# Kernel tuning notes

Hardware: AMD Instinct MI355X
Metric: run time of the kernel (lower is better)

## Reference

```python
import jax, jax.numpy as jnp
import numpy as np

C = 1.0          # curvature of PoincareBall
SQRT_C = 1.0
MIN_NORM = 1e-15
PROJ_EPS = 4e-3  # float32 boundary eps used by PoincareBall.proj
N_NODES = 50000


def _norm(x):
    return jnp.clip(jnp.linalg.norm(x, axis=-1, keepdims=True), MIN_NORM)


def _artanh(x):
    return jnp.arctanh(jnp.clip(x, -1.0 + 1e-7, 1.0 - 1e-7))


def proj(x):
    # clip points to the open ball of radius (1-eps)/sqrt(c)
    norm = _norm(x)
    maxnorm = (1.0 - PROJ_EPS) / SQRT_C
    return jnp.where(norm > maxnorm, x / norm * maxnorm, x)


def expmap0(u):
    u_norm = _norm(u)
    return jnp.tanh(SQRT_C * u_norm) * u / (SQRT_C * u_norm)


def logmap0(p):
    p_norm = _norm(p)
    return _artanh(SQRT_C * p_norm) * p / (SQRT_C * p_norm)


def mobius_add(x, y):
    x2 = jnp.sum(x * x, -1, keepdims=True)
    y2 = jnp.sum(y * y, -1, keepdims=True)
    xy = jnp.sum(x * y, -1, keepdims=True)
    num = (1.0 + 2.0 * C * xy + C * y2) * x + (1.0 - C * x2) * y
    den = 1.0 + 2.0 * C * xy + C * C * x2 * y2
    return num / jnp.clip(den, MIN_NORM)


def mobius_matvec(m, x):
    x_norm = _norm(x)
    mx = x @ m.T  # [N, d_out]
    mx_norm = _norm(mx)
    res = jnp.tanh(mx_norm / x_norm * _artanh(SQRT_C * x_norm)) * mx / (mx_norm * SQRT_C)
    zero_row = jnp.all(mx == 0, axis=-1, keepdims=True)
    return jnp.where(zero_row, jnp.zeros_like(res), res)


def setup_inputs() -> dict:
    key = jax.random.key(0)
    k = jax.random.split(key, 6)
    n, d_in, d_out, n_edges = N_NODES, 256, 96, 800000
    # points on the Poincare ball
    x = proj(0.02 * jax.random.normal(k[0], (n, d_in), jnp.float32))
    weight = jax.random.normal(k[1], (d_out, d_in), jnp.float32) * (1.0 / np.sqrt(d_in)).astype(np.float32)
    bias = jax.random.normal(k[2], (d_out,), jnp.float32) * 0.01
    edge_row = jax.random.randint(k[3], (n_edges,), 0, n)
    edge_col = jax.random.randint(k[4], (n_edges,), 0, n)
    # normalized adjacency weights ~ 1/avg_degree
    edge_weight = jax.random.uniform(k[5], (n_edges,), jnp.float32) * (1.0 / 16.0)
    return {"x": x, "weight": weight, "bias": bias, "edge_weight": edge_weight,
            "edge_row": edge_row, "edge_col": edge_col}


def reference(x, weight, bias, edge_weight, edge_row, edge_col):
    # --- HypLinear (dropout inactive in eval) ---
    h = proj(mobius_matvec(weight, x))
    hyp_bias = proj(expmap0(bias[None, :]))  # proj_tan0 is identity on the ball
    h = proj(mobius_add(h, hyp_bias))
    # --- HypAgg: spmm(adj, logmap0(h)) then expmap0 ---
    xt = logmap0(h)                                  # [N, d_out]
    msgs = edge_weight[:, None] * xt[edge_col]       # [E, d_out]
    support = jax.ops.segment_sum(msgs, edge_row, num_segments=N_NODES)
    h = proj(expmap0(support))
    # --- HypAct: relu in tangent space, map back (c_in == c_out) ---
    h = proj(expmap0(jax.nn.relu(logmap0(h))))
    return h
```

## Files before the change

kernel.cpp:

```cpp
#include <hip/hip_runtime.h>


typedef __attribute__((ext_vector_type(8))) short short8;
typedef __attribute__((ext_vector_type(4))) float floatx4;

#define DIN 256
#define DOUT 96
#define MAXN 0.996f
#define EPS15 1e-15f
#define ATC (1.0f - 1e-7f)
#define NBK 391
#define CAP 3072
#define TILE 3072

__device__ __forceinline__ float us2f(unsigned short u) {
    unsigned int v = ((unsigned int)u) << 16;
    return __uint_as_float(v);
}
__device__ __forceinline__ unsigned short f2us(float f) {
    unsigned int b = __float_as_uint(f);
    unsigned int r = (b + 0x7FFFu + ((b >> 16) & 1u)) >> 16;
    return (unsigned short)r;
}

__global__ void initzero_kernel(const unsigned short* __restrict__ xraw,
                                const void* __restrict__ bias,
                                const void* __restrict__ wgt,
                                float* __restrict__ ws,
                                int* __restrict__ gcur) {
    int i = blockIdx.x * blockDim.x + threadIdx.x;
    int stride = gridDim.x * blockDim.x;
    for (int k = i; k < NBK * 16; k += stride) gcur[k] = 0;

    if (blockIdx.x == 0 && threadIdx.x < 64) {
        int l = threadIdx.x;
        float v0 = us2f(xraw[l]);
        float v1 = us2f(xraw[64 + l]);
        int big = (!(fabsf(v0) < 1e4f)) || (!(fabsf(v1) < 1e4f));
        #pragma unroll
        for (int m = 32; m >= 1; m >>= 1) big |= __shfl_xor(big, m, 64);
        bool isb = !big;
        if (l == 0) ws[97] = isb ? 1.0f : 0.0f;

        float b0 = isb ? us2f(((const unsigned short*)bias)[l])
                       : ((const float*)bias)[l];
        float b1 = 0.0f;
        if (l < 32)
            b1 = isb ? us2f(((const unsigned short*)bias)[64 + l])
                     : ((const float*)bias)[64 + l];
        float n2 = b0 * b0 + b1 * b1;
        #pragma unroll
        for (int m = 32; m >= 1; m >>= 1) n2 += __shfl_xor(n2, m, 64);
        float bn = fmaxf(sqrtf(n2), EPS15);
        float ef = tanhf(bn) / bn;
        float hn = ef * sqrtf(n2);
        float s = (hn > MAXN) ? MAXN / fmaxf(hn, EPS15) : 1.0f;
        ws[l] = s * ef * b0;
        if (l < 32) ws[64 + l] = s * ef * b1;
        if (l == 0) { float v = s * hn; ws[96] = v * v; }
    }

    if (blockIdx.x >= 1 && blockIdx.x <= 12) {
        int t = threadIdx.x, lane = t & 63;
        float v0 = us2f(xraw[lane]);
        float v1 = us2f(xraw[64 + lane]);
        int big = (!(fabsf(v0) < 1e4f)) || (!(fabsf(v1) < 1e4f));
        #pragma unroll
        for (int m = 32; m >= 1; m >>= 1) big |= __shfl_xor(big, m, 64);
        bool isb = !big;
        uint4* wz = (uint4*)(ws + 128);
        int g = t + 256 * (int)(blockIdx.x - 1);
        int c = g >> 5, j = g & 31;
        int f = c >> 4, mr = c & 15;
        int kt = j >> 2, q = j & 3;
        if (isb) {
            const uint4* wg = (const uint4*)wgt;
            wz[(f * 8 + kt) * 64 + q * 16 + mr] = wg[g];
        } else {
            const float* wgf = (const float*)wgt;
            const float* src = wgf + (size_t)c * DIN + j * 8;
            unsigned short tmp[8];
            #pragma unroll
            for (int z = 0; z < 8; z++) tmp[z] = f2us(src[z]);
            wz[(f * 8 + kt) * 64 + q * 16 + mr] = *(const uint4*)tmp;
        }
    }
}

__global__ void __launch_bounds__(256) parthyp_kernel(
        const void* __restrict__ x,
        const void* __restrict__ ew,
        const int* __restrict__ erow,
        const int* __restrict__ ecol,
        float* __restrict__ ws,
        int* __restrict__ gcur,
        uint2* __restrict__ arena,
        unsigned short* __restrict__ xtb,
        int N, int E, int Pb) {
    __shared__ int sh_h[NBK], sh_c[NBK], sh_g[NBK];

    const int t = threadIdx.x;
    const bool isb = ws[97] != 0.0f;

    int b = blockIdx.x;
    bool ispart; int idx;
    if (b < 2 * Pb) { ispart = (b & 1); idx = b >> 1; }
    else            { ispart = false;   idx = b - Pb; }

    if (ispart) {
        const int tb = idx * TILE;

        for (int i = t; i < NBK; i += 256) { sh_h[i] = 0; sh_c[i] = 0; }
        __syncthreads();

        int rw[12]; unsigned int pk[12];
        #pragma unroll
        for (int k = 0; k < 12; k++) {
            int e = tb + t + 256 * k;
            if (e < E) {
                int r = erow[e];
                unsigned int wb = isb ? (unsigned int)((const unsigned short*)ew)[e]
                                      : (unsigned int)f2us(((const float*)ew)[e]);
                rw[k] = r;
                pk[k] = (wb << 16) | (unsigned int)ecol[e];
                atomicAdd(&sh_h[r >> 7], 1);
            } else rw[k] = -1;
        }
        __syncthreads();

        for (int b2 = t; b2 < NBK; b2 += 256)
            sh_g[b2] = atomicAdd(&gcur[b2 * 16], sh_h[b2]);
        __syncthreads();

        #pragma unroll
        for (int k = 0; k < 12; k++) {
            if (rw[k] >= 0) {
                int b2 = rw[k] >> 7;
                int p = sh_g[b2] + atomicAdd(&sh_c[b2], 1);
                if (p < CAP)
                    arena[(size_t)b2 * CAP + p] =
                        make_uint2(pk[k], (unsigned int)rw[k]);
            }
        }
        return;
    }

    const int lane = t & 63;
    const int wv = t >> 6;
    const int mrow = lane & 15;
    const int quad = lane >> 4;
    const uint4* __restrict__ Wg = (const uint4*)(ws + 128);

    const int r0 = (idx * 4 + wv) * 16;
    if (r0 >= N) return;

    float hbl[6];
    #pragma unroll
    for (int f = 0; f < 6; f++) hbl[f] = ws[mrow + 16 * f];
    const float hb2 = ws[96];

    int xr = r0 + mrow; if (xr >= N) xr = N - 1;
    short8 afrag[8];
    if (isb) {
        const unsigned short* xrow = (const unsigned short*)x + (size_t)xr * DIN + quad * 8;
        #pragma unroll
        for (int kt = 0; kt < 8; kt++)
            afrag[kt] = *(const short8*)(xrow + kt * 32);
    } else {
        const float* xrow = (const float*)x + (size_t)xr * DIN + quad * 8;
        #pragma unroll
        for (int kt = 0; kt < 8; kt++) {
            short8 a;
            #pragma unroll
            for (int j = 0; j < 8; j++) a[j] = (short)f2us(xrow[kt * 32 + j]);
            afrag[kt] = a;
        }
    }

    float xn2p = 0.f;
    #pragma unroll
    for (int kt = 0; kt < 8; kt++)
        #pragma unroll
        for (int j = 0; j < 8; j++) {
            float v = us2f((unsigned short)afrag[kt][j]);
            xn2p = fmaf(v, v, xn2p);
        }
    xn2p += __shfl_xor(xn2p, 16, 64);
    xn2p += __shfl_xor(xn2p, 32, 64);

    floatx4 acc[6];
    #pragma unroll
    for (int f = 0; f < 6; f++) acc[f] = (floatx4){0.f, 0.f, 0.f, 0.f};
    #pragma unroll
    for (int f = 0; f < 6; f++) {
        uint4 bw[8];
        #pragma unroll
        for (int kt = 0; kt < 8; kt++)
            bw[kt] = Wg[(f * 8 + kt) * 64 + lane];
        #pragma unroll
        for (int kt = 0; kt < 8; kt++) {
            short8 bfr = *(const short8*)&bw[kt];
            acc[f] = __builtin_amdgcn_mfma_f32_16x16x32_bf16(afrag[kt], bfr, acc[f], 0, 0, 0);
        }
    }

    float mxn2[4], dmh[4];
    #pragma unroll
    for (int reg = 0; reg < 4; reg++) {
        float a2 = 0.f, ad = 0.f;
        #pragma unroll
        for (int f = 0; f < 6; f++) {
            float v = acc[f][reg];
            a2 = fmaf(v, v, a2);
            ad = fmaf(v, hbl[f], ad);
        }
        mxn2[reg] = a2; dmh[reg] = ad;
    }
    #pragma unroll
    for (int m = 8; m >= 1; m >>= 1)
        #pragma unroll
        for (int reg = 0; reg < 4; reg++) {
            mxn2[reg] += __shfl_xor(mxn2[reg], m, 64);
            dmh[reg]  += __shfl_xor(dmh[reg],  m, 64);
        }

    int sel = mrow & 3;
    float xn2  = __shfl(xn2p, quad * 4 + sel, 64);
    float wmx2 = mxn2[sel], wdmh = dmh[sel];

    float xn  = fmaxf(sqrtf(xn2), EPS15);
    float mxn = fmaxf(sqrtf(wmx2), EPS15);
    float g   = (mxn / xn) * atanhf(fminf(xn, ATC));
    float tg  = tanhf(g);
    float rs0 = tg / mxn;
    float rn  = rs0 * sqrtf(wmx2);
    float s1  = (rn > MAXN) ? MAXN / fmaxf(rn, EPS15) : 1.0f;
    float al  = s1 * rs0;
    float x2  = al * al * wmx2;
    float xy  = al * wdmh;
    float cA  = 1.0f + 2.0f * xy + hb2;
    float cB  = 1.0f - x2;
    float den = fmaxf(1.0f + 2.0f * xy + x2 * hb2, EPS15);
    float p   = cA * al / den;
    float qq  = cB / den;
    float o2  = p*p*wmx2 + 2.0f*p*qq*wdmh + qq*qq*hb2;
    float on  = sqrtf(fmaxf(o2, 0.0f));
    float s2  = (on > MAXN) ? MAXN / fmaxf(on, EPS15) : 1.0f;
    float pn  = fmaxf(s2 * on, EPS15);
    float F   = (atanhf(fminf(pn, ATC)) / pn) * s2;
    float Fp_m = F * p, Fq_m = F * qq;

    float Fp[4], Fq[4];
    #pragma unroll
    for (int reg = 0; reg < 4; reg++) {
        Fp[reg] = __shfl(Fp_m, quad * 16 + reg, 64);
        Fq[reg] = __shfl(Fq_m, quad * 16 + reg, 64);
    }

    #pragma unroll
    for (int reg = 0; reg < 4; reg++) {
        int row = r0 + quad * 4 + reg;
        if (row < N) {
            size_t base = (size_t)row * DOUT + mrow;
            #pragma unroll
            for (int f = 0; f < 6; f++)
                xtb[base + 16 * f] = f2us(fmaf(Fp[reg], acc[f][reg], Fq[reg] * hbl[f]));
        }
    }
}

__global__ void __launch_bounds__(256) sortg_kernel(
        const int* __restrict__ gcur,
        uint2* __restrict__ arena,
        uint2* __restrict__ roff) {
    __shared__ int h[128], h8[128], excl[128], cur[128];

    const int t = threadIdx.x;
    const int idx = blockIdx.x;
    int cnt = gcur[idx * 16]; if (cnt > CAP) cnt = CAP;
    const size_t ab = (size_t)idx * CAP;

    for (int i = t; i < 128; i += 256) h[i] = 0;
    __syncthreads();

    uint2 ent[12];
    #pragma unroll
    for (int k = 0; k < 12; k++) {
        int j = t + 256 * k;
        if (j < cnt) {
            ent[k] = arena[ab + j];
            atomicAdd(&h[ent[k].y & 127u], 1);
        } else ent[k] = make_uint2(0u, 0u);
    }
    __syncthreads();

    if (t < 64) {
        int a0 = h[2 * t], a1 = h[2 * t + 1];
        int p0 = (a0 + 7) & ~7, p1 = (a1 + 7) & ~7;
        int ps = p0 + p1;
        int sc = ps;
        #pragma unroll
        for (int d = 1; d < 64; d <<= 1) {
            int tt = __shfl_up(sc, d, 64);
            if (t >= d) sc += tt;
        }
        int ex = sc - ps;
        h8[2 * t] = p0;        h8[2 * t + 1] = p1;
        excl[2 * t] = ex;      excl[2 * t + 1] = ex + p0;
        cur[2 * t]  = ex;      cur[2 * t + 1]  = ex + p0;
    }
    __syncthreads();

    if (t < 128) {
        int e8 = excl[t];
        int c8 = h8[t];
        if (e8 > CAP) e8 = CAP;
        if (e8 + c8 > CAP) c8 = CAP - e8;
        if (c8 < 0) c8 = 0;
        roff[idx * 128 + t] =
            make_uint2((unsigned int)(ab + e8), (unsigned int)c8);
        for (int j = excl[t] + h[t]; j < excl[t] + h8[t]; j++)
            if (j < CAP) arena[ab + j] = make_uint2(0u, 0u);
    }
    #pragma unroll
    for (int k = 0; k < 12; k++) {
        int j = t + 256 * k;
        if (j < cnt) {
            int slot = atomicAdd(&cur[ent[k].y & 127u], 1);
            if (slot < CAP)
                arena[ab + slot] =
                    make_uint2((ent[k].x & 0xFFFFu) * 192u,
                               ent[k].x & 0xFFFF0000u);
        }
    }
}

__global__ void __launch_bounds__(256) rowagg_kernel(
        const unsigned short* __restrict__ xtb,
        const uint2* __restrict__ arena,
        const uint2* __restrict__ roff,
        const float* __restrict__ ws,
        void* __restrict__ out, int N) {
    int wv = threadIdx.x >> 6, lane = threadIdx.x & 63;
    int node = blockIdx.x * 4 + wv;
    if (node >= N) return;
    const bool isb = ws[97] != 0.0f;
    const bool act = lane < 48;

    uint2 ro = roff[node];
    unsigned int start = ro.x;
    int cnt8 = (int)ro.y;

    const char* __restrict__ xc = (const char*)xtb;
    const unsigned int lsel = act ? (unsigned int)lane * 4u : 0u;

    float acc0 = 0.f, acc1 = 0.f;
    unsigned int uA[8], uB[8];
    float wA[8], wB[8];

#define ISSUE(BU, BW, B)                                                       \
    _Pragma("unroll")                                                          \
    for (int k = 0; k < 8; k++) {                                              \
        int idx = (B) * 8 + k;                                                 \
        unsigned int off = (unsigned int)__shfl((int)my.x, idx, 64);           \
        BW[k] = __uint_as_float((unsigned int)__shfl((int)my.y, idx, 64));     \
        BU[k] = *(const unsigned int*)(xc + off + lsel);                       \
    }

#define CONSUME(BU, BW)                                                        \
    _Pragma("unroll")                                                          \
    for (int k = 0; k < 8; k++) {                                              \
        acc0 = fmaf(BW[k], __uint_as_float(BU[k] << 16), acc0);                \
        acc1 = fmaf(BW[k], __uint_as_float(BU[k] & 0xFFFF0000u), acc1);        \
    }

    for (int cs = 0; cs < cnt8; cs += 64) {
        int navail = cnt8 - cs; if (navail > 64) navail = 64;
        uint2 my = arena[start + cs + lane];
        int nb = navail >> 3;
        ISSUE(uA, wA, 0);
        for (int bb = 1; bb < nb; bb++) {
            if (bb & 1) { ISSUE(uB, wB, bb); CONSUME(uA, wA); }
            else        { ISSUE(uA, wA, bb); CONSUME(uB, wB); }
        }
        if (nb & 1) { CONSUME(uA, wA); }
        else        { CONSUME(uB, wB); }
    }
#undef ISSUE
#undef CONSUME

    if (!act) { acc0 = 0.f; acc1 = 0.f; }

    float u0 = acc0, u1 = acc1;
    float n2 = u0*u0 + u1*u1;
    #pragma unroll
    for (int m = 32; m >= 1; m >>= 1) n2 += __shfl_xor(n2, m, 64);
    float un = fmaxf(sqrtf(n2), EPS15);
    float ef = tanhf(un) / un;
    float p0 = ef * u0, p1 = ef * u1;
    float pnrm = ef * sqrtf(n2);
    float sc = (pnrm > MAXN) ? MAXN / fmaxf(pnrm, EPS15) : 1.0f;
    p0 *= sc; p1 *= sc; pnrm *= sc;
    float pncl = fmaxf(pnrm, EPS15);
    float lf = atanhf(fminf(pncl, ATC)) / pncl;
    float t0 = fmaxf(lf * p0, 0.0f), t1 = fmaxf(lf * p1, 0.0f);
    float tn2 = t0*t0 + t1*t1;
    #pragma unroll
    for (int m = 32; m >= 1; m >>= 1) tn2 += __shfl_xor(tn2, m, 64);
    float tn = fmaxf(sqrtf(tn2), EPS15);
    float ef2 = tanhf(tn) / tn;
    float en = ef2 * sqrtf(tn2);
    float s2 = (en > MAXN) ? MAXN / fmaxf(en, EPS15) : 1.0f;
    float scale = s2 * ef2;
    float v0 = scale * t0, v1 = scale * t1;

    if (act) {
        if (isb) {
            unsigned int pk = ((unsigned int)f2us(v1) << 16) | (unsigned int)f2us(v0);
            ((unsigned int*)((unsigned short*)out + (size_t)node * DOUT))[lane] = pk;
        } else {
            float2 fv; fv.x = v0; fv.y = v1;
            ((float2*)((float*)out + (size_t)node * DOUT))[lane] = fv;
        }
    }
}

extern "C" void kernel_launch(void* const* d_in, const int* in_sizes, int n_in,
                              void* d_out, int out_size, void* d_ws, size_t ws_size,
                              hipStream_t stream) {
    const void* x    = d_in[0];
    const void* wgt  = d_in[1];
    const void* bias = d_in[2];
    const void* ew   = d_in[3];
    const int* erow  = (const int*)d_in[4];
    const int* ecol  = (const int*)d_in[5];

    int N = out_size / DOUT;
    int E = in_sizes[4];

    float* wsf = (float*)d_ws;
    int* gcur = (int*)(wsf + 128 + 12288);
    uint2* arena = (uint2*)((char*)d_ws + 74688);
    unsigned short* xtb = (unsigned short*)((char*)d_ws + 74688 + (size_t)NBK * CAP * 8);
    uint2* roff = (uint2*)(xtb + (size_t)N * DOUT);

    int Pb = (E + TILE - 1) / TILE;
    int Hb = (N + 63) / 64;

    initzero_kernel<<<13, 256, 0, stream>>>((const unsigned short*)x, bias, wgt, wsf, gcur);
    parthyp_kernel<<<Pb + Hb, 256, 0, stream>>>(x, ew, erow, ecol, wsf, gcur,
                                                arena, xtb, N, E, Pb);
    sortg_kernel<<<NBK, 256, 0, stream>>>(gcur, arena, roff);
    rowagg_kernel<<<(N + 3) / 4, 256, 0, stream>>>(xtb, arena, roff, wsf, d_out, N);
}
```

Baseline: 171.9 us.

## Use fast transcendental intrinsics and uniform edge loads in row aggregation

Replaces the library tanh, atanh, sqrt and divisions with hardware exp2, log, rcp and sqrt intrinsics plus small-argument polynomials, in both the matvec epilogue and the aggregation epilogue. The row aggregation loop now reads edge entries directly through a wave-uniform pointer (readfirstlane on the row offset and count) instead of loading 64 entries per lane and broadcasting each through shuffles. The aim is to cut ALU and cross-lane shuffle work in both kernels, at the cost of reduced accuracy in the transcendentals.

```diff
diff --git a/kernel.cpp b/kernel.cpp
--- a/kernel.cpp
+++ b/kernel.cpp
@@ -21,6 +21,22 @@
     unsigned int b = __float_as_uint(f);
     unsigned int r = (b + 0x7FFFu + ((b >> 16) & 1u)) >> 16;
     return (unsigned short)r;
+}
+
+__device__ __forceinline__ float ftanh(float x) {
+    float xc = fminf(x, 15.0f);
+    float e = __builtin_amdgcn_exp2f(xc * 2.8853900817779268f);
+    float big = (e - 1.0f) * __builtin_amdgcn_rcpf(e + 1.0f);
+    float x2 = x * x;
+    float small = x * fmaf(x2, fmaf(x2, 0.13333334f, -0.33333334f), 1.0f);
+    return (x < 0.04f) ? small : big;
+}
+__device__ __forceinline__ float fatanh(float x) {
+    float r = 2.0f * x * __builtin_amdgcn_rcpf(1.0f - x);
+    float big = __builtin_amdgcn_logf(1.0f + r) * 0.34657359028f;
+    float x2 = x * x;
+    float small = x * fmaf(x2, fmaf(x2, 0.2f, 0.33333334f), 1.0f);
+    return (x < 0.04f) ? small : big;
 }
 
 __global__ void initzero_kernel(const unsigned short* __restrict__ xraw,
@@ -228,26 +244,26 @@
     float xn2  = __shfl(xn2p, quad * 4 + sel, 64);
     float wmx2 = mxn2[sel], wdmh = dmh[sel];
 
-    float xn  = fmaxf(sqrtf(xn2), EPS15);
-    float mxn = fmaxf(sqrtf(wmx2), EPS15);
-    float g   = (mxn / xn) * atanhf(fminf(xn, ATC));
-    float tg  = tanhf(g);
-    float rs0 = tg / mxn;
-    float rn  = rs0 * sqrtf(wmx2);
-    float s1  = (rn > MAXN) ? MAXN / fmaxf(rn, EPS15) : 1.0f;
+    float xn  = fmaxf(__builtin_amdgcn_sqrtf(xn2), EPS15);
+    float mxn = fmaxf(__builtin_amdgcn_sqrtf(wmx2), EPS15);
+    float g   = mxn * __builtin_amdgcn_rcpf(xn) * fatanh(fminf(xn, ATC));
+    float tg  = ftanh(g);
+    float rs0 = tg * __builtin_amdgcn_rcpf(mxn);
+    float rn  = rs0 * __builtin_amdgcn_sqrtf(wmx2);
+    float s1  = (rn > MAXN) ? MAXN * __builtin_amdgcn_rcpf(fmaxf(rn, EPS15)) : 1.0f;
     float al  = s1 * rs0;
     float x2  = al * al * wmx2;
     float xy  = al * wdmh;
     float cA  = 1.0f + 2.0f * xy + hb2;
     float cB  = 1.0f - x2;
-    float den = fmaxf(1.0f + 2.0f * xy + x2 * hb2, EPS15);
-    float p   = cA * al / den;
-    float qq  = cB / den;
+    float rden = __builtin_amdgcn_rcpf(fmaxf(1.0f + 2.0f * xy + x2 * hb2, EPS15));
+    float p   = cA * al * rden;
+    float qq  = cB * rden;
     float o2  = p*p*wmx2 + 2.0f*p*qq*wdmh + qq*qq*hb2;
-    float on  = sqrtf(fmaxf(o2, 0.0f));
-    float s2  = (on > MAXN) ? MAXN / fmaxf(on, EPS15) : 1.0f;
+    float on  = __builtin_amdgcn_sqrtf(fmaxf(o2, 0.0f));
+    float s2  = (on > MAXN) ? MAXN * __builtin_amdgcn_rcpf(fmaxf(on, EPS15)) : 1.0f;
     float pn  = fmaxf(s2 * on, EPS15);
-    float F   = (atanhf(fminf(pn, ATC)) / pn) * s2;
+    float F   = fatanh(fminf(pn, ATC)) * __builtin_amdgcn_rcpf(pn) * s2;
     float Fp_m = F * p, Fq_m = F * qq;
 
     float Fp[4], Fq[4];
@@ -348,46 +364,46 @@
     const bool act = lane < 48;
 
     uint2 ro = roff[node];
-    unsigned int start = ro.x;
-    int cnt8 = (int)ro.y;
+    unsigned int start = (unsigned int)__builtin_amdgcn_readfirstlane((int)ro.x);
+    int cnt8 = __builtin_amdgcn_readfirstlane((int)ro.y);
+    const uint2* __restrict__ ap = arena + start;
 
     const char* __restrict__ xc = (const char*)xtb;
     const unsigned int lsel = act ? (unsigned int)lane * 4u : 0u;
 
     float acc0 = 0.f, acc1 = 0.f;
+    uint2 eA[8], eB[8];
     unsigned int uA[8], uB[8];
-    float wA[8], wB[8];
-
-#define ISSUE(BU, BW, B)                                                       \
+
+#define SLOAD(EE, J)                                                           \
+    _Pragma("unroll")                                                          \
+    for (int k = 0; k < 8; k++) EE[k] = ap[(J) + k];
+
+#define GATHER(UU, EE)                                                         \
+    _Pragma("unroll")                                                          \
+    for (int k = 0; k < 8; k++)                                                \
+        UU[k] = *(const unsigned int*)(xc + EE[k].x + lsel);
+
+#define CONS(UU, EE)                                                           \
     _Pragma("unroll")                                                          \
     for (int k = 0; k < 8; k++) {                                              \
-        int idx = (B) * 8 + k;                                                 \
-        unsigned int off = (unsigned int)__shfl((int)my.x, idx, 64);           \
-        BW[k] = __uint_as_float((unsigned int)__shfl((int)my.y, idx, 64));     \
-        BU[k] = *(const unsigned int*)(xc + off + lsel);                       \
-    }
-
-#define CONSUME(BU, BW)                                                        \
-    _Pragma("unroll")                                                          \
-    for (int k = 0; k < 8; k++) {                                              \
-        acc0 = fmaf(BW[k], __uint_as_float(BU[k] << 16), acc0);                \
-        acc1 = fmaf(BW[k], __uint_as_float(BU[k] & 0xFFFF0000u), acc1);        \
-    }
-
-    for (int cs = 0; cs < cnt8; cs += 64) {
-        int navail = cnt8 - cs; if (navail > 64) navail = 64;
-        uint2 my = arena[start + cs + lane];
-        int nb = navail >> 3;
-        ISSUE(uA, wA, 0);
-        for (int bb = 1; bb < nb; bb++) {
-            if (bb & 1) { ISSUE(uB, wB, bb); CONSUME(uA, wA); }
-            else        { ISSUE(uA, wA, bb); CONSUME(uB, wB); }
-        }
-        if (nb & 1) { CONSUME(uA, wA); }
-        else        { CONSUME(uB, wB); }
-    }
-#undef ISSUE
-#undef CONSUME
+        float w = __uint_as_float(EE[k].y);                                    \
+        acc0 = fmaf(w, __uint_as_float(UU[k] << 16), acc0);                    \
+        acc1 = fmaf(w, __uint_as_float(UU[k] & 0xFFFF0000u), acc1);            \
+    }
+
+    if (cnt8 > 0) {
+        SLOAD(eA, 0); GATHER(uA, eA);
+        for (int j = 8; j < cnt8; j += 8) {
+            if ((j >> 3) & 1) { SLOAD(eB, j); GATHER(uB, eB); CONS(uA, eA); }
+            else              { SLOAD(eA, j); GATHER(uA, eA); CONS(uB, eB); }
+        }
+        if ((cnt8 >> 3) & 1) { CONS(uA, eA); }
+        else                 { CONS(uB, eB); }
+    }
+#undef SLOAD
+#undef GATHER
+#undef CONS
 
     if (!act) { acc0 = 0.f; acc1 = 0.f; }
 
@@ -395,22 +411,22 @@
     float n2 = u0*u0 + u1*u1;
     #pragma unroll
     for (int m = 32; m >= 1; m >>= 1) n2 += __shfl_xor(n2, m, 64);
-    float un = fmaxf(sqrtf(n2), EPS15);
-    float ef = tanhf(un) / un;
+    float un = fmaxf(__builtin_amdgcn_sqrtf(n2), EPS15);
+    float ef = ftanh(un) * __builtin_amdgcn_rcpf(un);
     float p0 = ef * u0, p1 = ef * u1;
-    float pnrm = ef * sqrtf(n2);
-    float sc = (pnrm > MAXN) ? MAXN / fmaxf(pnrm, EPS15) : 1.0f;
+    float pnrm = ef * __builtin_amdgcn_sqrtf(n2);
+    float sc = (pnrm > MAXN) ? MAXN * __builtin_amdgcn_rcpf(fmaxf(pnrm, EPS15)) : 1.0f;
     p0 *= sc; p1 *= sc; pnrm *= sc;
     float pncl = fmaxf(pnrm, EPS15);
-    float lf = atanhf(fminf(pncl, ATC)) / pncl;
+    float lf = fatanh(fminf(pncl, ATC)) * __builtin_amdgcn_rcpf(pncl);
     float t0 = fmaxf(lf * p0, 0.0f), t1 = fmaxf(lf * p1, 0.0f);
     float tn2 = t0*t0 + t1*t1;
     #pragma unroll
     for (int m = 32; m >= 1; m >>= 1) tn2 += __shfl_xor(tn2, m, 64);
-    float tn = fmaxf(sqrtf(tn2), EPS15);
-    float ef2 = tanhf(tn) / tn;
-    float en = ef2 * sqrtf(tn2);
-    float s2 = (en > MAXN) ? MAXN / fmaxf(en, EPS15) : 1.0f;
+    float tn = fmaxf(__builtin_amdgcn_sqrtf(tn2), EPS15);
+    float ef2 = ftanh(tn) * __builtin_amdgcn_rcpf(tn);
+    float en = ef2 * __builtin_amdgcn_sqrtf(tn2);
+    float s2 = (en > MAXN) ? MAXN * __builtin_amdgcn_rcpf(fmaxf(en, EPS15)) : 1.0f;
     float scale = s2 * ef2;
     float v0 = scale * t0, v1 = scale * t1;
 
```

Result: faster. 159.5 us (-7.2%).
